# Performance work log

Measured on AMD Instinct MI355X. Metric: run time of the kernel, lower is better.

Reference implementation:

```python
import jax, jax.numpy as jnp
import numpy as np
from jax.scipy.stats import norm
from jax.scipy.special import ndtri

B, S, F = 512, 2048, 128

def setup_inputs() -> dict:
    key = jax.random.key(0)
    k1, k2, k3 = jax.random.split(key, 3)
    x = jax.random.normal(k1, (B, F), dtype=jnp.float32)
    cdf_data = jax.random.normal(k2, (S, F), dtype=jnp.float32)
    bw_param = jax.random.uniform(k3, (1, F), dtype=jnp.float32)
    return {"x": x, "cdf_data": cdf_data, "bw_param": bw_param}

def reference(x, cdf_data, bw_param):
    # trainable bandwidths: bw = sigmoid(raw param), shape [1, F]
    bw = jax.nn.sigmoid(bw_param)[0]  # [F]
    # Pairwise Gaussian-CDF KDE: for each (b, f), mean over stored samples s of
    # Phi((x[b,f] - cdf_data[s,f]) / bw[f]).  Intermediate z: [B, S, F].
    z = (x[:, None, :] - cdf_data[None, :, :]) / bw  # [B, S, F]
    u = jnp.mean(norm.cdf(z), axis=1)               # [B, F], uniform-ish in (0,1)
    # normal_backtransform=True: map uniform -> standard normal via inverse CDF
    return ndtri(u)
```

## Files before the change

kernel.cpp:

```cpp
#include <hip/hip_runtime.h>
#include <math.h>

#define FDIM  128
#define SDIM  2048
#define BDIM  512
#define GPTS  32
#define NCH   32
#define CHUNK (SDIM / NCH)
#define NT    1024
#define BG    256
#define NBLK  (FDIM * (BDIM / BG))
#define XMIN  (-6.0)
#define XSPAN (12.0)

__device__ __forceinline__ double ndtri_pair(double u, double cu) {
    double q = u - 0.5;
    if (fabs(q) <= 0.425) {
        double r = 0.180625 - q * q;
        double num = (((((((2.5090809287301226727e3  * r + 3.3430575583588128105e4) * r +
                            6.7265770927008700853e4) * r + 4.5921953931549871457e4) * r +
                            1.3731693765509461125e4) * r + 1.9715909503065514427e3) * r +
                            1.3314166789178437745e2) * r + 3.3871328727963666080e0);
        double den = (((((((5.2264952788528545610e3  * r + 2.8729085735721942674e4) * r +
                            3.9307895800092710610e4) * r + 2.1213794301586595867e4) * r +
                            5.3941960214247511077e3) * r + 6.8718700749205790830e2) * r +
                            4.2313330701600911252e1) * r + 1.0);
        return q * num / den;
    }
    double r = (q < 0.0) ? u : cu;
    r = fmax(r, 1e-300);
    r = sqrt(-log(r));
    double val;
    if (r <= 5.0) {
        r -= 1.6;
        double num = (((((((7.74545014278341407640e-4 * r + 2.27238449892691845833e-2) * r +
                            2.41780725177450611770e-1) * r + 1.27045825245236838258e0) * r +
                            3.64784832476320460504e0)  * r + 5.76949722146069140550e0) * r +
                            4.63033784615654529590e0)  * r + 1.42343711074968357734e0);
        double den = (((((((1.05075007164441684324e-9 * r + 5.47593808499534494600e-4) * r +
                            1.51986665636164571966e-2) * r + 1.48103976427480074590e-1) * r +
                            6.89767334985100004550e-1) * r + 1.67638483018380384940e0) * r +
                            2.05319162663775882187e0)  * r + 1.0);
        val = num / den;
    } else {
        r -= 5.0;
        double num = (((((((2.01033439929228813265e-7 * r + 2.71155556874348757815e-5) * r +
                            1.24266094738807843860e-3) * r + 2.65321895265761230930e-2) * r +
                            2.96560571828504891230e-1) * r + 1.78482653991729133580e0) * r +
                            5.46378491116411436990e0)  * r + 6.65790464350110377720e0);
        double den = (((((((2.04426310338993978564e-15 * r + 1.42151175831644588870e-7) * r +
                            1.84631831751005468180e-5)  * r + 7.86869131145613259100e-4) * r +
                            1.48753612908506148525e-2)  * r + 1.36929880922735805310e-1) * r +
                            5.99832206555887937690e-1)  * r + 1.0);
        val = num / den;
    }
    return (q < 0.0) ? -val : val;
}

__global__ __launch_bounds__(NT) void fused_kernel(
    const float* __restrict__ x, const float* __restrict__ cdf,
    const float* __restrict__ bwp, float* __restrict__ out)
{
    const int blk = blockIdx.x;
    const int f   = blk >> 1;
    const int bg  = blk & 1;
    const int B0  = bg * BG;
    const int tid = threadIdx.x;

    __shared__ float2 spart[NCH][GPTS];
    __shared__ double tab[GPTS][3];

    {
        const int g  = tid & (GPTS - 1);
        const int ch = tid >> 5;

        const float p = bwp[f];
        const float s = (1.0f + __expf(-p)) * 0.70710678118654752f;
        const float c1s    = 0.3275911f * s;
        const float negs2l = -(s * s) * 1.4426950408889634f;
        const float xg = (float)(XMIN + (double)g * (XSPAN / (GPTS - 1)));

        const float* cp = cdf + (size_t)(ch * CHUNK) * FDIM + f;

        float acc0 = 0.f, acc1 = 0.f, acc2 = 0.f, acc3 = 0.f;
        float dac = 0.f;

        #pragma unroll 2
        for (int i = 0; i < CHUNK; i += 4) {
            float c0 = cp[0 * FDIM];
            float c1 = cp[1 * FDIM];
            float c2 = cp[2 * FDIM];
            float c3 = cp[3 * FDIM];
            cp += 4 * FDIM;

            float d0 = xg - c0, d1 = xg - c1, d2 = xg - c2, d3 = xg - c3;

            float t0 = __builtin_amdgcn_rcpf(fmaf(c1s, fabsf(d0), 1.0f));
            float t1 = __builtin_amdgcn_rcpf(fmaf(c1s, fabsf(d1), 1.0f));
            float t2 = __builtin_amdgcn_rcpf(fmaf(c1s, fabsf(d2), 1.0f));
            float t3 = __builtin_amdgcn_rcpf(fmaf(c1s, fabsf(d3), 1.0f));

            float x0 = exp2f(d0 * d0 * negs2l);
            float x1 = exp2f(d1 * d1 * negs2l);
            float x2 = exp2f(d2 * d2 * negs2l);
            float x3 = exp2f(d3 * d3 * negs2l);

            float q0 = fmaf(0.53070271450f, t0, -0.72657601350f);
            float q1 = fmaf(0.53070271450f, t1, -0.72657601350f);
            float q2 = fmaf(0.53070271450f, t2, -0.72657601350f);
            float q3 = fmaf(0.53070271450f, t3, -0.72657601350f);
            q0 = fmaf(q0, t0, 0.71070687050f);  q1 = fmaf(q1, t1, 0.71070687050f);
            q2 = fmaf(q2, t2, 0.71070687050f);  q3 = fmaf(q3, t3, 0.71070687050f);
            q0 = fmaf(q0, t0, -0.14224836800f); q1 = fmaf(q1, t1, -0.14224836800f);
            q2 = fmaf(q2, t2, -0.14224836800f); q3 = fmaf(q3, t3, -0.14224836800f);
            q0 = fmaf(q0, t0, 0.12741479600f);  q1 = fmaf(q1, t1, 0.12741479600f);
            q2 = fmaf(q2, t2, 0.12741479600f);  q3 = fmaf(q3, t3, 0.12741479600f);

            float e0 = q0 * t0 * x0;
            float e1 = q1 * t1 * x1;
            float e2 = q2 * t2 * x2;
            float e3 = q3 * t3 * x3;

            acc0 += (d0 >= 0.f) ? (1.0f - e0) : e0;
            acc1 += (d1 >= 0.f) ? (1.0f - e1) : e1;
            acc2 += (d2 >= 0.f) ? (1.0f - e2) : e2;
            acc3 += (d3 >= 0.f) ? (1.0f - e3) : e3;
            dac  += (x0 + x1) + (x2 + x3);
        }

        spart[ch][g] = make_float2((acc0 + acc1) + (acc2 + acc3), dac);
    }
    __syncthreads();

    if (tid < GPTS) {
        double a = 0.0, da = 0.0;
        #pragma unroll
        for (int ch = 0; ch < NCH; ++ch) {
            float2 v = spart[ch][tid];
            a  += (double)v.x;
            da += (double)v.y;
        }
        const double invS = 1.0 / (double)SDIM;
        const double invbw = 1.0 + exp(-(double)bwp[f]);
        tab[tid][0] = a * invS;
        tab[tid][1] = ((double)SDIM - a) * invS;
        tab[tid][2] = da * invbw * (invS / 2.5066282746310002);
    }
    __syncthreads();

    if (tid < BG) {
        const int idx = (B0 + tid) * FDIM + f;

        const double H = XSPAN / (GPTS - 1);
        double t = ((double)x[idx] - XMIN) * ((GPTS - 1) / XSPAN);
        t = fmin(fmax(t, 0.0), (double)(GPTS - 1));
        int i = (int)t;
        if (i > GPTS - 2) i = GPTS - 2;
        double w = t - (double)i;

        double u0 = tab[i][0],     u1 = tab[i + 1][0];
        double c0 = tab[i][1],     c1 = tab[i + 1][1];
        double m0 = tab[i][2],     m1 = tab[i + 1][2];

        double w2 = w * w, w3 = w2 * w;
        double h00 = 2.0 * w3 - 3.0 * w2 + 1.0;
        double h10 = w3 - 2.0 * w2 + w;
        double h01 = 3.0 * w2 - 2.0 * w3;
        double h11 = w3 - w2;
        double dterm = H * (h10 * m0 + h11 * m1);
        double u  = h00 * u0 + h01 * u1 + dterm;
        double cu = h00 * c0 + h01 * c1 - dterm;

        out[idx] = (float)ndtri_pair(u, cu);
    }
}

extern "C" void kernel_launch(void* const* d_in, const int* in_sizes, int n_in,
                              void* d_out, int out_size, void* d_ws, size_t ws_size,
                              hipStream_t stream) {
    const float* x   = (const float*)d_in[0];
    const float* cdf = (const float*)d_in[1];
    const float* bwp = (const float*)d_in[2];
    float* out = (float*)d_out;

    fused_kernel<<<dim3(NBLK), dim3(NT), 0, stream>>>(x, cdf, bwp, out);
}
```

Baseline: 71.43 us.

## Split fused KDE kernel into chunked table build and interpolation kernels

Splits the single fused kernel into two launches. The first builds per-chunk partial CDF tables, with each block staging a 16-sample slice of cdf_data in shared memory and computing all features for 16 grid points. Partials go to workspace, and the second kernel reduces them with shuffles and does the Hermite interpolation plus ndtri. The original kernel computed the table twice per feature (once per batch half) and read cdf with strided loads. The new layout removes that redundant table work and coalesces the loads, at the cost of a second launch and a workspace round-trip.

```diff
diff --git a/kernel.cpp b/kernel.cpp
--- a/kernel.cpp
+++ b/kernel.cpp
@@ -5,11 +5,11 @@
 #define SDIM  2048
 #define BDIM  512
 #define GPTS  32
-#define NCH   32
-#define CHUNK (SDIM / NCH)
-#define NT    1024
-#define BG    256
-#define NBLK  (FDIM * (BDIM / BG))
+#define NCHK  128
+#define CSZ   (SDIM / NCHK)
+#define NT1   1024
+#define NT2   256
+#define BG2   256
 #define XMIN  (-6.0)
 #define XSPAN (12.0)
 
@@ -57,122 +57,132 @@
     return (q < 0.0) ? -val : val;
 }
 
-__global__ __launch_bounds__(NT) void fused_kernel(
-    const float* __restrict__ x, const float* __restrict__ cdf,
-    const float* __restrict__ bwp, float* __restrict__ out)
+__device__ __forceinline__ void eval1(float d, float c1s, float negs2l,
+                                      float& acc, float& dac) {
+    float t  = __builtin_amdgcn_rcpf(fmaf(c1s, fabsf(d), 1.0f));
+    float ex = exp2f(d * d * negs2l);
+    float q  = fmaf(0.53070271450f, t, -0.72657601350f);
+    q = fmaf(q, t, 0.71070687050f);
+    q = fmaf(q, t, -0.14224836800f);
+    q = fmaf(q, t, 0.12741479600f);
+    float e = q * t * ex;
+    acc += (d >= 0.f) ? (1.0f - e) : e;
+    dac += ex;
+}
+
+__global__ __launch_bounds__(NT1) void table_kernel(
+    const float* __restrict__ cdf, const float* __restrict__ bwp,
+    float2* __restrict__ part)
 {
-    const int blk = blockIdx.x;
-    const int f   = blk >> 1;
-    const int bg  = blk & 1;
-    const int B0  = bg * BG;
+    const int c   = blockIdx.x >> 1;
+    const int h   = blockIdx.x & 1;
     const int tid = threadIdx.x;
-
-    __shared__ float2 spart[NCH][GPTS];
+    const int f   = tid & (FDIM - 1);
+    const int gq  = tid >> 7;
+
+    __shared__ float sc[CSZ][FDIM];
+
+    {
+        const float4* src = reinterpret_cast<const float4*>(
+            cdf + (size_t)c * CSZ * FDIM);
+        float4* dst = reinterpret_cast<float4*>(&sc[0][0]);
+        if (tid < 512) dst[tid] = src[tid];
+    }
+    __syncthreads();
+
+    const float p = bwp[f];
+    const float s = (1.0f + __expf(-p)) * 0.70710678118654752f;
+    const float c1s    = 0.3275911f * s;
+    const float negs2l = -(s * s) * 1.4426950408889634f;
+
+    const int g0 = h * 16 + gq;
+    const int g1 = g0 + 8;
+    const float xg0 = (float)(XMIN + (double)g0 * (XSPAN / (GPTS - 1)));
+    const float xg1 = (float)(XMIN + (double)g1 * (XSPAN / (GPTS - 1)));
+
+    float a0 = 0.f, da0 = 0.f, a1 = 0.f, da1 = 0.f;
+    #pragma unroll
+    for (int s2 = 0; s2 < CSZ; s2 += 2) {
+        float cA = sc[s2][f];
+        float cB = sc[s2 + 1][f];
+        eval1(xg0 - cA, c1s, negs2l, a0, da0);
+        eval1(xg0 - cB, c1s, negs2l, a0, da0);
+        eval1(xg1 - cA, c1s, negs2l, a1, da1);
+        eval1(xg1 - cB, c1s, negs2l, a1, da1);
+    }
+
+    part[((size_t)(f * GPTS + g0)) * NCHK + c] = make_float2(a0, da0);
+    part[((size_t)(f * GPTS + g1)) * NCHK + c] = make_float2(a1, da1);
+}
+
+__global__ __launch_bounds__(NT2) void interp_kernel(
+    const float* __restrict__ x, const float* __restrict__ bwp,
+    const float2* __restrict__ part, float* __restrict__ out)
+{
+    const int f   = blockIdx.x >> 1;
+    const int bg  = blockIdx.x & 1;
+    const int B0  = bg * BG2;
+    const int tid = threadIdx.x;
+
+    __shared__ float2 sl[GPTS * NCHK];
     __shared__ double tab[GPTS][3];
 
     {
-        const int g  = tid & (GPTS - 1);
-        const int ch = tid >> 5;
-
-        const float p = bwp[f];
-        const float s = (1.0f + __expf(-p)) * 0.70710678118654752f;
-        const float c1s    = 0.3275911f * s;
-        const float negs2l = -(s * s) * 1.4426950408889634f;
-        const float xg = (float)(XMIN + (double)g * (XSPAN / (GPTS - 1)));
-
-        const float* cp = cdf + (size_t)(ch * CHUNK) * FDIM + f;
-
-        float acc0 = 0.f, acc1 = 0.f, acc2 = 0.f, acc3 = 0.f;
-        float dac = 0.f;
-
-        #pragma unroll 2
-        for (int i = 0; i < CHUNK; i += 4) {
-            float c0 = cp[0 * FDIM];
-            float c1 = cp[1 * FDIM];
-            float c2 = cp[2 * FDIM];
-            float c3 = cp[3 * FDIM];
-            cp += 4 * FDIM;
-
-            float d0 = xg - c0, d1 = xg - c1, d2 = xg - c2, d3 = xg - c3;
-
-            float t0 = __builtin_amdgcn_rcpf(fmaf(c1s, fabsf(d0), 1.0f));
-            float t1 = __builtin_amdgcn_rcpf(fmaf(c1s, fabsf(d1), 1.0f));
-            float t2 = __builtin_amdgcn_rcpf(fmaf(c1s, fabsf(d2), 1.0f));
-            float t3 = __builtin_amdgcn_rcpf(fmaf(c1s, fabsf(d3), 1.0f));
-
-            float x0 = exp2f(d0 * d0 * negs2l);
-            float x1 = exp2f(d1 * d1 * negs2l);
-            float x2 = exp2f(d2 * d2 * negs2l);
-            float x3 = exp2f(d3 * d3 * negs2l);
-
-            float q0 = fmaf(0.53070271450f, t0, -0.72657601350f);
-            float q1 = fmaf(0.53070271450f, t1, -0.72657601350f);
-            float q2 = fmaf(0.53070271450f, t2, -0.72657601350f);
-            float q3 = fmaf(0.53070271450f, t3, -0.72657601350f);
-            q0 = fmaf(q0, t0, 0.71070687050f);  q1 = fmaf(q1, t1, 0.71070687050f);
-            q2 = fmaf(q2, t2, 0.71070687050f);  q3 = fmaf(q3, t3, 0.71070687050f);
-            q0 = fmaf(q0, t0, -0.14224836800f); q1 = fmaf(q1, t1, -0.14224836800f);
-            q2 = fmaf(q2, t2, -0.14224836800f); q3 = fmaf(q3, t3, -0.14224836800f);
-            q0 = fmaf(q0, t0, 0.12741479600f);  q1 = fmaf(q1, t1, 0.12741479600f);
-            q2 = fmaf(q2, t2, 0.12741479600f);  q3 = fmaf(q3, t3, 0.12741479600f);
-
-            float e0 = q0 * t0 * x0;
-            float e1 = q1 * t1 * x1;
-            float e2 = q2 * t2 * x2;
-            float e3 = q3 * t3 * x3;
-
-            acc0 += (d0 >= 0.f) ? (1.0f - e0) : e0;
-            acc1 += (d1 >= 0.f) ? (1.0f - e1) : e1;
-            acc2 += (d2 >= 0.f) ? (1.0f - e2) : e2;
-            acc3 += (d3 >= 0.f) ? (1.0f - e3) : e3;
-            dac  += (x0 + x1) + (x2 + x3);
-        }
-
-        spart[ch][g] = make_float2((acc0 + acc1) + (acc2 + acc3), dac);
+        const float4* src = reinterpret_cast<const float4*>(
+            part + (size_t)f * GPTS * NCHK);
+        float4* dst = reinterpret_cast<float4*>(sl);
+        #pragma unroll
+        for (int k = tid; k < 2048; k += NT2) dst[k] = src[k];
     }
     __syncthreads();
 
-    if (tid < GPTS) {
+    {
+        const int g = tid >> 3;
+        const int k = tid & 7;
         double a = 0.0, da = 0.0;
         #pragma unroll
-        for (int ch = 0; ch < NCH; ++ch) {
-            float2 v = spart[ch][tid];
+        for (int j = 0; j < NCHK / 8; ++j) {
+            float2 v = sl[g * NCHK + j * 8 + k];
             a  += (double)v.x;
             da += (double)v.y;
         }
-        const double invS = 1.0 / (double)SDIM;
-        const double invbw = 1.0 + exp(-(double)bwp[f]);
-        tab[tid][0] = a * invS;
-        tab[tid][1] = ((double)SDIM - a) * invS;
-        tab[tid][2] = da * invbw * (invS / 2.5066282746310002);
+        for (int m = 1; m < 8; m <<= 1) {
+            a  += __shfl_xor(a, m, 64);
+            da += __shfl_xor(da, m, 64);
+        }
+        if (k == 0) {
+            const double invS = 1.0 / (double)SDIM;
+            const double invbw = 1.0 + exp(-(double)bwp[f]);
+            tab[g][0] = a * invS;
+            tab[g][1] = ((double)SDIM - a) * invS;
+            tab[g][2] = da * invbw * (invS / 2.5066282746310002);
+        }
     }
     __syncthreads();
 
-    if (tid < BG) {
-        const int idx = (B0 + tid) * FDIM + f;
-
-        const double H = XSPAN / (GPTS - 1);
-        double t = ((double)x[idx] - XMIN) * ((GPTS - 1) / XSPAN);
-        t = fmin(fmax(t, 0.0), (double)(GPTS - 1));
-        int i = (int)t;
-        if (i > GPTS - 2) i = GPTS - 2;
-        double w = t - (double)i;
-
-        double u0 = tab[i][0],     u1 = tab[i + 1][0];
-        double c0 = tab[i][1],     c1 = tab[i + 1][1];
-        double m0 = tab[i][2],     m1 = tab[i + 1][2];
-
-        double w2 = w * w, w3 = w2 * w;
-        double h00 = 2.0 * w3 - 3.0 * w2 + 1.0;
-        double h10 = w3 - 2.0 * w2 + w;
-        double h01 = 3.0 * w2 - 2.0 * w3;
-        double h11 = w3 - w2;
-        double dterm = H * (h10 * m0 + h11 * m1);
-        double u  = h00 * u0 + h01 * u1 + dterm;
-        double cu = h00 * c0 + h01 * c1 - dterm;
-
-        out[idx] = (float)ndtri_pair(u, cu);
-    }
+    const int idx = (B0 + tid) * FDIM + f;
+
+    const double H = XSPAN / (GPTS - 1);
+    double t = ((double)x[idx] - XMIN) * ((GPTS - 1) / XSPAN);
+    t = fmin(fmax(t, 0.0), (double)(GPTS - 1));
+    int i = (int)t;
+    if (i > GPTS - 2) i = GPTS - 2;
+    double w = t - (double)i;
+
+    double u0 = tab[i][0],     u1 = tab[i + 1][0];
+    double c0 = tab[i][1],     c1 = tab[i + 1][1];
+    double m0 = tab[i][2],     m1 = tab[i + 1][2];
+
+    double w2 = w * w, w3 = w2 * w;
+    double h00 = 2.0 * w3 - 3.0 * w2 + 1.0;
+    double h10 = w3 - 2.0 * w2 + w;
+    double h01 = 3.0 * w2 - 2.0 * w3;
+    double h11 = w3 - w2;
+    double dterm = H * (h10 * m0 + h11 * m1);
+    double u  = h00 * u0 + h01 * u1 + dterm;
+    double cu = h00 * c0 + h01 * c1 - dterm;
+
+    out[idx] = (float)ndtri_pair(u, cu);
 }
 
 extern "C" void kernel_launch(void* const* d_in, const int* in_sizes, int n_in,
@@ -183,5 +193,8 @@
     const float* bwp = (const float*)d_in[2];
     float* out = (float*)d_out;
 
-    fused_kernel<<<dim3(NBLK), dim3(NT), 0, stream>>>(x, cdf, bwp, out);
-}
+    float2* part = (float2*)d_ws;
+
+    table_kernel<<<dim3(NCHK * 2), dim3(NT1), 0, stream>>>(cdf, bwp, part);
+    interp_kernel<<<dim3(FDIM * 2), dim3(NT2), 0, stream>>>(x, bwp, part, out);
+}
```

Result: no change. 72.37 us (+1.3%).
